# Kernel optimization log

Hardware: AMD Instinct MI355X
Metric: run time of the kernel (lower is better)

## Reference

```python
import jax, jax.numpy as jnp
import numpy as np

K, NR, NT, D, NLAYER = 128, 1, 128, 1, 8
PMAX = float(np.power(10.0, 10.0 / 10.0))  # snr=10 dB
SIGMA = 1.0


def _cx(x):
    # [2, ...] real/imag-stacked -> complex
    return x[0] + 1j * x[1]


def _ct(x):
    # conjugate transpose on last two axes
    return jnp.conj(jnp.swapaxes(x, -1, -2))


def _layer(Vc, Hc, up1, up3, up4, wp1, wp3, vp1, vp2, vp4):
    # Vc: [K,Nt,d] complex, Hc: [K,Nr,Nt] complex; params complex, batched over K.
    cdt = Vc.dtype
    I_nr = jnp.eye(NR, dtype=cdt)
    I_d = jnp.eye(D, dtype=cdt)
    I_nt = jnp.eye(NT, dtype=cdt)
    # ---- A_update: A_i = sigma/Pmax * sum_j tr(V_j V_j^H) * I + H_i (sum_j V_j V_j^H) H_i^H
    tr_vv = jnp.einsum('knd,knd->', Vc, jnp.conj(Vc))          # complex scalar
    S = jnp.einsum('knd,kmd->nm', Vc, jnp.conj(Vc))            # [Nt,Nt]
    A = (SIGMA / PMAX) * tr_vv * I_nr + jnp.einsum('krt,tm,ksm->krs', Hc, S, jnp.conj(Hc))  # [K,Nr,Nr]
    # ---- U layer: A_inv_i = p1_i inv(A_i) + 0.01 p3_i ; U_i = A_inv_i H_i V_i + p4_i
    A_inv = up1 @ jnp.linalg.inv(A) + 0.01 * up3
    Un = A_inv @ Hc @ Vc + up4                                  # [K,Nr,d]
    # ---- E_update: E_i = I - U_i^H H_i V_i
    E = I_d - _ct(Un) @ Hc @ Vc                                 # [K,d,d]
    # ---- W layer: W_i = 0.1 p1_i inv(E_i) + 0.01 p3_i
    Wn = 0.1 * (wp1 @ jnp.linalg.inv(E)) + 0.01 * wp3           # [K,d,d]
    # ---- B_update: B = sigma/Pmax * sum_i tr(U_i W_i U_i^H) * I + sum_i H_i^H U_i W_i U_i^H H_i (same for all users)
    UWU = Un @ Wn @ _ct(Un)                                     # [K,Nr,Nr]
    tr_uwu = jnp.trace(UWU, axis1=-2, axis2=-1).sum()
    B = (SIGMA / PMAX) * tr_uwu * I_nt + jnp.sum(_ct(Hc) @ UWU @ Hc, axis=0)  # [Nt,Nt]
    B_inv = jnp.linalg.inv(B)
    # ---- V
    if vp2 is None:  # FinalV: V_i = inv(B) H_i^H U_i W_i
        Vn = (B_inv @ _ct(Hc)) @ Un @ Wn
    else:            # V layer: B_inv_i = p2_i inv(B) + 0.01 p4_i ; V_i = B_inv_i H_i^H U_i W_i + p1_i
        Bm = vp2 @ B_inv + 0.01 * vp4
        Vn = Bm @ _ct(Hc) @ Un @ Wn + vp1
    # ---- Normalize: scale by sqrt(Pmax)/sqrt(Re sum_j tr(V_j V_j^H))
    pw = jnp.sqrt(jnp.real(jnp.einsum('knd,knd->', Vn, jnp.conj(Vn))))
    return (jnp.sqrt(PMAX) / pw) * Vn


def setup_inputs() -> dict:
    key = jax.random.key(0)
    ks = jax.random.split(key, 20)
    f32 = jnp.float32
    def rn(k, shape, scale):
        return (scale * jax.random.normal(k, shape)).astype(f32)
    inp = {
        'V': rn(ks[0], (2, K, NT, D), 1.0),
        'H': rn(ks[1], (2, K, NR, NT), 1.0),
        # mid-layer params, stacked over layers: only params actually used in forward
        'mid_u_p1': rn(ks[2], (NLAYER, 2, K, NR, NR), 0.001),
        'mid_u_p3': rn(ks[3], (NLAYER, 2, K, NR, NR), 0.01),
        'mid_u_p4': rn(ks[4], (NLAYER, 2, K, NR, D), 0.01),
        'mid_w_p1': rn(ks[5], (NLAYER, 2, K, D, D), 0.001),
        'mid_w_p3': rn(ks[6], (NLAYER, 2, K, D, D), 0.01),
        'mid_v_p1': rn(ks[7], (NLAYER, 2, K, NT, D), 0.001),
        'mid_v_p2': rn(ks[8], (NLAYER, 2, K, NT, NT), 0.01),
        'mid_v_p4': rn(ks[9], (NLAYER, 2, K, NT, NT), 0.01),
        # final layer (U + W only)
        'fin_u_p1': rn(ks[10], (2, K, NR, NR), 0.001),
        'fin_u_p3': rn(ks[11], (2, K, NR, NR), 0.01),
        'fin_u_p4': rn(ks[12], (2, K, NR, D), 0.01),
        'fin_w_p1': rn(ks[13], (2, K, D, D), 0.001),
        'fin_w_p3': rn(ks[14], (2, K, D, D), 0.01),
    }
    return inp


def reference(V, H, mid_u_p1, mid_u_p3, mid_u_p4, mid_w_p1, mid_w_p3,
              mid_v_p1, mid_v_p2, mid_v_p4,
              fin_u_p1, fin_u_p3, fin_u_p4, fin_w_p1, fin_w_p3):
    Vc = _cx(V)
    Hc = _cx(H)
    n = mid_u_p1.shape[0]
    for l in range(n):
        Vc = _layer(Vc, Hc,
                    _cx(mid_u_p1[l]), _cx(mid_u_p3[l]), _cx(mid_u_p4[l]),
                    _cx(mid_w_p1[l]), _cx(mid_w_p3[l]),
                    _cx(mid_v_p1[l]), _cx(mid_v_p2[l]), _cx(mid_v_p4[l]))
    Vc = _layer(Vc, Hc,
                _cx(fin_u_p1), _cx(fin_u_p3), _cx(fin_u_p4),
                _cx(fin_w_p1), _cx(fin_w_p3), None, None, None)
    return jnp.stack([jnp.real(Vc), jnp.imag(Vc)]).astype(jnp.float32)
```

## Files before the change

kernel.cpp:

```cpp
#include <hip/hip_runtime.h>
#include <math.h>

#define KK 128
#define NTT 128
#define PMAXF 10.0f
#define SP 0.1f
#define LDA2 130

typedef float2 c32;

__device__ __forceinline__ c32 cmul(c32 a, c32 b){
    return make_float2(a.x*b.x - a.y*b.y, a.x*b.y + a.y*b.x);
}
__device__ __forceinline__ c32 cmulc(c32 a, c32 b){
    return make_float2(a.x*b.x + a.y*b.y, a.y*b.x - a.x*b.y);
}
__device__ __forceinline__ c32 cinv(c32 a){
    float d = 1.0f/(a.x*a.x + a.y*a.y);
    return make_float2(a.x*d, -a.y*d);
}

__global__ void k_trvv(const float* __restrict__ V0, float* __restrict__ out){
    float s = 0.f;
    for (int e = blockIdx.x*blockDim.x + threadIdx.x; e < 2*KK*NTT; e += gridDim.x*blockDim.x){
        float v = V0[e]; s += v*v;
    }
    __shared__ float red[4];
    for (int d = 32; d; d >>= 1) s += __shfl_down(s, d);
    int lane = threadIdx.x & 63, w = threadIdx.x >> 6;
    if (!lane) red[w] = s;
    __syncthreads();
    if (!threadIdx.x){
        float t = red[0] + red[1] + red[2] + red[3];
        atomicAdd(out, t);
    }
}

__global__ void k_stage1(const float* __restrict__ Hre, const float* __restrict__ Him,
                         const float* __restrict__ V0re, const float* __restrict__ V0im,
                         const float2* __restrict__ VN, int use_vn,
                         const float* __restrict__ pw2prev,
                         const float* __restrict__ trvvp,
                         const float* __restrict__ u1, const float* __restrict__ u3,
                         const float* __restrict__ u4, const float* __restrict__ w1,
                         const float* __restrict__ w3,
                         float* __restrict__ wre, float* __restrict__ wim,
                         float* __restrict__ sre, float* __restrict__ sim,
                         float* __restrict__ sumw)
{
    int k = blockIdx.x, j = threadIdx.x;
    __shared__ float hre_s[NTT], him_s[NTT];
    __shared__ float redq[NTT];
    __shared__ c32 pkk_s;
    hre_s[j] = Hre[k*NTT + j];
    him_s[j] = Him[k*NTT + j];
    __syncthreads();

    float g = 1.0f;
    if (pw2prev) g = sqrtf(PMAXF / *pw2prev);

    float pre = 0.f, pim = 0.f;
    if (use_vn){
        const float2* vr = VN + j*NTT;
        #pragma unroll 4
        for (int n = 0; n < NTT; n++){
            float2 v = vr[n];
            pre += hre_s[n]*v.x - him_s[n]*v.y;
            pim += hre_s[n]*v.y + him_s[n]*v.x;
        }
    } else {
        const float* vr = V0re + j*NTT;
        const float* vi = V0im + j*NTT;
        #pragma unroll 4
        for (int n = 0; n < NTT; n++){
            float a = vr[n], b = vi[n];
            pre += hre_s[n]*a - him_s[n]*b;
            pim += hre_s[n]*b + him_s[n]*a;
        }
    }
    pre *= g; pim *= g;
    if (j == k) pkk_s = make_float2(pre, pim);
    redq[j] = pre*pre + pim*pim;
    __syncthreads();
    for (int d = 64; d; d >>= 1){
        if (j < d) redq[j] += redq[j + d];
        __syncthreads();
    }
    if (j == 0){
        float trvv = pw2prev ? PMAXF : *trvvp;
        float A = SP*trvv + redq[0];
        float invA = 1.0f/A;
        c32 p1 = make_float2(u1[k], u1[KK + k]);
        c32 p3 = make_float2(u3[k], u3[KK + k]);
        c32 p4 = make_float2(u4[k], u4[KK + k]);
        c32 Ainv = make_float2(p1.x*invA + 0.01f*p3.x, p1.y*invA + 0.01f*p3.y);
        c32 Pkk = pkk_s;
        c32 U = cmul(Ainv, Pkk); U.x += p4.x; U.y += p4.y;
        c32 t = cmulc(Pkk, U);
        c32 E = make_float2(1.0f - t.x, -t.y);
        c32 iE = cinv(E);
        c32 q1 = make_float2(w1[k], w1[KK + k]);
        c32 q3 = make_float2(w3[k], w3[KK + k]);
        c32 W = cmul(q1, iE);
        W.x = 0.1f*W.x + 0.01f*q3.x;
        W.y = 0.1f*W.y + 0.01f*q3.y;
        float u2 = U.x*U.x + U.y*U.y;
        c32 wk = make_float2(u2*W.x, u2*W.y);
        c32 sk = cmul(U, W);
        wre[k] = wk.x; wim[k] = wk.y;
        sre[k] = sk.x; sim[k] = sk.y;
        atomicAdd(&sumw[0], wk.x);
        atomicAdd(&sumw[1], wk.y);
    }
}

__global__ void k_bbuild(const float* __restrict__ Hre, const float* __restrict__ Him,
                         const float* __restrict__ wre, const float* __restrict__ wim,
                         const float* __restrict__ sumw, float2* __restrict__ B)
{
    int n = blockIdx.x, m = threadIdx.x;
    __shared__ float cr[KK], ci[KK];
    {
        int k = m;
        c32 h = make_float2(Hre[k*NTT + n], -Him[k*NTT + n]);
        c32 wk = make_float2(wre[k], wim[k]);
        c32 t = cmul(h, wk);
        cr[k] = t.x; ci[k] = t.y;
    }
    __syncthreads();
    float br = 0.f, bi = 0.f;
    #pragma unroll 4
    for (int k = 0; k < KK; k++){
        float hr = Hre[k*NTT + m], hi = Him[k*NTT + m];
        br += cr[k]*hr - ci[k]*hi;
        bi += cr[k]*hi + ci[k]*hr;
    }
    if (n == m){ br += SP*sumw[0]; bi += SP*sumw[1]; }
    B[n*NTT + m] = make_float2(br, bi);
}

__global__ void __launch_bounds__(512, 1) k_lu12(const float2* __restrict__ B,
                                                 float2* __restrict__ BT,
                                                 float2* __restrict__ rcg,
                                                 int* __restrict__ permg,
                                                 const float* __restrict__ p4re,
                                                 const float* __restrict__ p4im,
                                                 const float* __restrict__ Hre,
                                                 const float* __restrict__ Him,
                                                 float2* __restrict__ Z)
{
    if (blockIdx.x > 0){
        int k = blockIdx.x - 1;
        int t = threadIdx.x;
        int r = t >> 2, q = t & 3;
        const float* mre = p4re + (size_t)k*16384 + (size_t)r*128 + q*32;
        const float* mim = p4im + (size_t)k*16384 + (size_t)r*128 + q*32;
        const float* hr4 = Hre + k*NTT + q*32;
        const float* hi4 = Him + k*NTT + q*32;
        float ar = 0.f, ai = 0.f;
        #pragma unroll
        for (int ii = 0; ii < 8; ++ii){
            float4 a = *(const float4*)(mre + 4*ii);
            float4 b = *(const float4*)(mim + 4*ii);
            float4 hr = *(const float4*)(hr4 + 4*ii);
            float4 hi = *(const float4*)(hi4 + 4*ii);
            ar += a.x*hr.x + b.x*hi.x;  ai += b.x*hr.x - a.x*hi.x;
            ar += a.y*hr.y + b.y*hi.y;  ai += b.y*hr.y - a.y*hi.y;
            ar += a.z*hr.z + b.z*hi.z;  ai += b.z*hr.z - a.z*hi.z;
            ar += a.w*hr.w + b.w*hi.w;  ai += b.w*hr.w - a.w*hi.w;
        }
        ar += __shfl_xor(ar, 1); ai += __shfl_xor(ai, 1);
        ar += __shfl_xor(ar, 2); ai += __shfl_xor(ai, 2);
        if (q == 0) Z[k*NTT + r] = make_float2(ar, ai);
        return;
    }

    extern __shared__ float2 As[];
    __shared__ float2 rc_s[KK];
    __shared__ float2 Us[16*17];
    __shared__ float2 MM[16*16];
    __shared__ float2 MscT[16*114];
    const int t = threadIdx.x;

    {
        const float4* B4 = (const float4*)B;
        float4* A4 = (float4*)As;
        for (int e = t; e < KK*64; e += 512){
            int r = e >> 6, cq = e & 63;
            A4[r*65 + cq] = B4[e];
        }
    }
    __syncthreads();

    for (int j = 0; j < 8; ++j){
        const int J0 = j*16, T0 = J0 + 16, Rt = 128 - T0;

        if (t < 64){
            if (t < 16){
                const int l = t;
                float2 d[16], rcr[16];
                #pragma unroll
                for (int h = 0; h < 8; ++h){
                    float4 q = *(const float4*)&As[(J0 + l)*LDA2 + J0 + 2*h];
                    d[2*h]   = make_float2(q.x, q.y);
                    d[2*h+1] = make_float2(q.z, q.w);
                }
                #pragma unroll
                for (int ii = 0; ii < 16; ++ii){
                    float2 piv;
                    piv.x = __shfl(d[ii].x, ii);
                    piv.y = __shfl(d[ii].y, ii);
                    float2 rc = cinv(piv);
                    rcr[ii] = rc;
                    if (l == ii) rc_s[J0 + ii] = rc;
                    float2 m = cmul(d[ii], rc);
                    const bool act = (l > ii);
                    #pragma unroll
                    for (int c = ii + 1; c < 16; ++c){
                        float ux = __shfl(d[c].x, ii);
                        float uy = __shfl(d[c].y, ii);
                        if (act){
                            d[c].x -= m.x*ux - m.y*uy;
                            d[c].y -= m.x*uy + m.y*ux;
                        }
                    }
                }
                #pragma unroll
                for (int h = 0; h < 8; ++h)
                    *(float4*)&As[(J0 + l)*LDA2 + J0 + 2*h] =
                        make_float4(d[2*h].x, d[2*h].y, d[2*h+1].x, d[2*h+1].y);
                #pragma unroll
                for (int c = 0; c < 16; ++c) Us[l*17 + c] = d[c];
                if (l >= 1){
                    #pragma unroll
                    for (int i = 0; i < 15; ++i){
                        if (i < l) MM[l*16 + i] = cmul(d[i], rcr[i]);
                    }
                }
            }
        } else if (j > 0){
            const int J0p = J0 - 16;
            const int ncp = (128 - T0) >> 1;
            int tt = t - 64;
            int cp = tt & 63, g = tt >> 6;
            if (cp < ncp){
                int c0 = T0 + 2*cp;
                float4 u2[16];
                #pragma unroll
                for (int i = 0; i < 16; ++i)
                    u2[i] = *(const float4*)&As[(J0p + i)*LDA2 + c0];
                int nb = (128 - J0) >> 1;
                for (int rb = g; rb < nb; rb += 7){
                    int r0_ = J0 + 2*rb;
                    float4 a0_ = *(const float4*)&As[r0_*LDA2 + c0];
                    float4 a1_ = *(const float4*)&As[(r0_ + 1)*LDA2 + c0];
                    #pragma unroll
                    for (int i = 0; i < 16; ++i){
                        float4 mm = *(const float4*)&MscT[i*114 + 2*rb];
                        float4 u = u2[i];
                        a0_.x -= mm.x*u.x - mm.y*u.y;  a0_.y -= mm.x*u.y + mm.y*u.x;
                        a0_.z -= mm.x*u.z - mm.y*u.w;  a0_.w -= mm.x*u.w + mm.y*u.z;
                        a1_.x -= mm.z*u.x - mm.w*u.y;  a1_.y -= mm.z*u.y + mm.w*u.x;
                        a1_.z -= mm.z*u.z - mm.w*u.w;  a1_.w -= mm.z*u.w + mm.w*u.z;
                    }
                    *(float4*)&As[r0_*LDA2 + c0] = a0_;
                    *(float4*)&As[(r0_ + 1)*LDA2 + c0] = a1_;
                }
            }
        }
        __syncthreads();

        if (j == 7) break;

        if (t < Rt){
            int c = T0 + t;
            float2 u[16];
            #pragma unroll
            for (int i = 0; i < 16; ++i) u[i] = As[(J0 + i)*LDA2 + c];
            #pragma unroll
            for (int a2 = 1; a2 < 16; ++a2){
                #pragma unroll
                for (int i = 0; i < 16; ++i){
                    if (i < a2){
                        float2 mm = MM[a2*16 + i];
                        u[a2].x -= mm.x*u[i].x - mm.y*u[i].y;
                        u[a2].y -= mm.x*u[i].y + mm.y*u[i].x;
                    }
                }
            }
            #pragma unroll
            for (int a2 = 1; a2 < 16; ++a2) As[(J0 + a2)*LDA2 + c] = u[a2];
        } else if (t >= 256 && t < 256 + Rt){
            int r = T0 + (t - 256);
            float2 v[16], tv[16];
            #pragma unroll
            for (int h = 0; h < 8; ++h){
                float4 q = *(const float4*)&As[r*LDA2 + J0 + 2*h];
                v[2*h]   = make_float2(q.x, q.y);
                v[2*h+1] = make_float2(q.z, q.w);
            }
            #pragma unroll
            for (int c = 0; c < 16; ++c){
                #pragma unroll
                for (int i = 0; i < 16; ++i){
                    if (i < c){
                        float2 uu = Us[i*17 + c];
                        float2 ti = tv[i];
                        v[c].x -= ti.x*uu.x - ti.y*uu.y;
                        v[c].y -= ti.x*uu.y + ti.y*uu.x;
                    }
                }
                tv[c] = cmul(v[c], rc_s[J0 + c]);
            }
            #pragma unroll
            for (int h = 0; h < 8; ++h)
                *(float4*)&As[r*LDA2 + J0 + 2*h] =
                    make_float4(v[2*h].x, v[2*h].y, v[2*h+1].x, v[2*h+1].y);
            int rp = r - T0;
            #pragma unroll
            for (int i = 0; i < 16; ++i) MscT[i*114 + rp] = tv[i];
        }
        __syncthreads();

        {
            int cp = t & 7, g = t >> 3;
            int c0 = T0 + 2*cp;
            float4 u2[16];
            #pragma unroll
            for (int i = 0; i < 16; ++i)
                u2[i] = *(const float4*)&As[(J0 + i)*LDA2 + c0];
            int nb = Rt >> 1;
            for (int rb = g; rb < nb; rb += 64){
                int r0_ = T0 + 2*rb;
                float4 a0_ = *(const float4*)&As[r0_*LDA2 + c0];
                float4 a1_ = *(const float4*)&As[(r0_ + 1)*LDA2 + c0];
                #pragma unroll
                for (int i = 0; i < 16; ++i){
                    float4 mm = *(const float4*)&MscT[i*114 + 2*rb];
                    float4 u = u2[i];
                    a0_.x -= mm.x*u.x - mm.y*u.y;  a0_.y -= mm.x*u.y + mm.y*u.x;
                    a0_.z -= mm.x*u.z - mm.y*u.w;  a0_.w -= mm.x*u.w + mm.y*u.z;
                    a1_.x -= mm.z*u.x - mm.w*u.y;  a1_.y -= mm.z*u.y + mm.w*u.x;
                    a1_.z -= mm.z*u.z - mm.w*u.w;  a1_.w -= mm.z*u.w + mm.w*u.z;
                }
                *(float4*)&As[r0_*LDA2 + c0] = a0_;
                *(float4*)&As[(r0_ + 1)*LDA2 + c0] = a1_;
            }
        }
        __syncthreads();
    }

    for (int e = t; e < KK*NTT; e += 512){
        int c = e >> 7, r = e & 127;
        BT[e] = As[r*LDA2 + c];
    }
    if (t < KK){ rcg[t] = rc_s[t]; permg[t] = t; }
}

__device__ __forceinline__ void solve_col(const float2* __restrict__ BT,
                                          const float2* __restrict__ rc_s,
                                          const int* __restrict__ permg,
                                          const float* __restrict__ Hre,
                                          const float* __restrict__ Him,
                                          int c, int lane, float2* __restrict__ xv)
{
    int r0 = lane, r1 = lane + 64;
    int o0 = permg[r0], o1 = permg[r1];
    float2 b0 = make_float2(Hre[c*NTT + o0], -Him[c*NTT + o0]);
    float2 b1 = make_float2(Hre[c*NTT + o1], -Him[c*NTT + o1]);

    float2 cur0[8], cur1[8];
    #pragma unroll
    for (int jj = 0; jj < 8; jj++){ cur0[jj] = BT[jj*NTT + r0]; cur1[jj] = BT[jj*NTT + r1]; }
    for (int ib = 0; ib < 16; ib++){
        float2 n0[8], n1[8];
        if (ib < 15){
            int nb = (ib + 1)*8;
            #pragma unroll
            for (int jj = 0; jj < 8; jj++){ n0[jj] = BT[(nb + jj)*NTT + r0]; n1[jj] = BT[(nb + jj)*NTT + r1]; }
        }
        #pragma unroll
        for (int jj = 0; jj < 8; jj++){
            int i = ib*8 + jj;
            float xr, xi;
            if (i < 64){ xr = __shfl(b0.x, i);      xi = __shfl(b0.y, i); }
            else       { xr = __shfl(b1.x, i - 64); xi = __shfl(b1.y, i - 64); }
            float2 rc = rc_s[i];
            float tr = rc.x*xr - rc.y*xi, ti = rc.x*xi + rc.y*xr;
            float2 l0 = cur0[jj], l1 = cur1[jj];
            if (r0 > i){ b0.x -= l0.x*tr - l0.y*ti; b0.y -= l0.x*ti + l0.y*tr; }
            if (r1 > i){ b1.x -= l1.x*tr - l1.y*ti; b1.y -= l1.x*ti + l1.y*tr; }
        }
        if (ib < 15){
            #pragma unroll
            for (int jj = 0; jj < 8; jj++){ cur0[jj] = n0[jj]; cur1[jj] = n1[jj]; }
        }
    }
    #pragma unroll
    for (int jj = 0; jj < 8; jj++){ cur0[jj] = BT[(120 + jj)*NTT + r0]; cur1[jj] = BT[(120 + jj)*NTT + r1]; }
    for (int ib = 15; ib >= 0; ib--){
        float2 n0[8], n1[8];
        if (ib > 0){
            int nb = (ib - 1)*8;
            #pragma unroll
            for (int jj = 0; jj < 8; jj++){ n0[jj] = BT[(nb + jj)*NTT + r0]; n1[jj] = BT[(nb + jj)*NTT + r1]; }
        }
        #pragma unroll
        for (int jj = 7; jj >= 0; jj--){
            int i = ib*8 + jj;
            float yr, yi;
            if (i < 64){ yr = __shfl(b0.x, i);      yi = __shfl(b0.y, i); }
            else       { yr = __shfl(b1.x, i - 64); yi = __shfl(b1.y, i - 64); }
            float2 rc = rc_s[i];
            float xr = rc.x*yr - rc.y*yi, xi = rc.x*yi + rc.y*yr;
            if (r0 == i){ b0.x = xr; b0.y = xi; }
            if (r1 == i){ b1.x = xr; b1.y = xi; }
            float2 u0 = cur0[jj], u1v = cur1[jj];
            if (r0 < i){ b0.x -= u0.x*xr - u0.y*xi; b0.y -= u0.x*xi + u0.y*xr; }
            if (r1 < i){ b1.x -= u1v.x*xr - u1v.y*xi; b1.y -= u1v.x*xi + u1v.y*xr; }
        }
        if (ib > 0){
            #pragma unroll
            for (int jj = 0; jj < 8; jj++){ cur0[jj] = n0[jj]; cur1[jj] = n1[jj]; }
        }
    }
    xv[r0] = b0;
    xv[r1] = b1;
}

__global__ void __launch_bounds__(512) k_solvemv(const float2* __restrict__ BT,
                                                 const float2* __restrict__ rcg,
                                                 const int* __restrict__ permg,
                                                 const float* __restrict__ Hre, const float* __restrict__ Him,
                                                 const float* __restrict__ p2re, const float* __restrict__ p2im,
                                                 const float2* __restrict__ Z,
                                                 const float* __restrict__ sre, const float* __restrict__ sim,
                                                 const float* __restrict__ p1re, const float* __restrict__ p1im,
                                                 float2* __restrict__ VN, float* __restrict__ pw2)
{
    int k = blockIdx.x;
    int t = threadIdx.x;
    __shared__ float2 xv[NTT];
    __shared__ float2 rc_s[KK];
    __shared__ float red[8];

    int r = t >> 2, q = t & 3;
    const float* mre = p2re + (size_t)k*16384 + (size_t)r*128 + q*32;
    const float* mim = p2im + (size_t)k*16384 + (size_t)r*128 + q*32;
    float4 pa[8], pb[8];
    #pragma unroll
    for (int ii = 0; ii < 8; ++ii){
        pa[ii] = *(const float4*)(mre + 4*ii);
        pb[ii] = *(const float4*)(mim + 4*ii);
    }
    if (t < 64){
        rc_s[t] = rcg[t];
        rc_s[t + 64] = rcg[t + 64];
        solve_col(BT, rc_s, permg, Hre, Him, k, t, xv);
    }
    __syncthreads();

    float ar = 0.f, ai = 0.f;
    #pragma unroll
    for (int ii = 0; ii < 8; ++ii){
        float4 a = pa[ii], b = pb[ii];
        float2 x0 = xv[q*32 + 4*ii], x1 = xv[q*32 + 4*ii + 1];
        float2 x2 = xv[q*32 + 4*ii + 2], x3 = xv[q*32 + 4*ii + 3];
        ar += a.x*x0.x - b.x*x0.y;  ai += a.x*x0.y + b.x*x0.x;
        ar += a.y*x1.x - b.y*x1.y;  ai += a.y*x1.y + b.y*x1.x;
        ar += a.z*x2.x - b.z*x2.y;  ai += a.z*x2.y + b.z*x2.x;
        ar += a.w*x3.x - b.w*x3.y;  ai += a.w*x3.y + b.w*x3.x;
    }
    ar += __shfl_xor(ar, 1); ai += __shfl_xor(ai, 1);
    ar += __shfl_xor(ar, 2); ai += __shfl_xor(ai, 2);
    float pwl = 0.f;
    if (q == 0){
        float2 z = Z[k*NTT + r];
        c32 s = make_float2(sre[k], sim[k]);
        float2 y = make_float2(ar + 0.01f*z.x, ai + 0.01f*z.y);
        c32 v = cmul(s, y);
        v.x += p1re[k*NTT + r]; v.y += p1im[k*NTT + r];
        VN[k*NTT + r] = v;
        pwl = v.x*v.x + v.y*v.y;
    }
    for (int d = 32; d; d >>= 1) pwl += __shfl_down(pwl, d);
    int lane = t & 63, w = t >> 6;
    if (!lane) red[w] = pwl;
    __syncthreads();
    if (!t){
        float tt = 0.f;
        #pragma unroll
        for (int w2 = 0; w2 < 8; ++w2) tt += red[w2];
        atomicAdd(pw2, tt);
    }
}

__global__ void __launch_bounds__(64) k_solvefin(const float2* __restrict__ BT,
                                                 const float2* __restrict__ rcg,
                                                 const int* __restrict__ permg,
                                                 const float* __restrict__ Hre, const float* __restrict__ Him,
                                                 const float* __restrict__ sre, const float* __restrict__ sim,
                                                 float2* __restrict__ VN, float* __restrict__ pw2)
{
    int c = blockIdx.x;
    int lane = threadIdx.x;
    __shared__ float2 xv[NTT];
    __shared__ float2 rc_s[KK];
    rc_s[lane] = rcg[lane];
    rc_s[lane + 64] = rcg[lane + 64];
    solve_col(BT, rc_s, permg, Hre, Him, c, lane, xv);

    c32 s = make_float2(sre[c], sim[c]);
    float2 v0 = cmul(s, xv[lane]);
    float2 v1 = cmul(s, xv[lane + 64]);
    VN[c*NTT + lane] = v0;
    VN[c*NTT + lane + 64] = v1;
    float pwl = v0.x*v0.x + v0.y*v0.y + v1.x*v1.x + v1.y*v1.y;
    for (int d = 32; d; d >>= 1) pwl += __shfl_down(pwl, d);
    if (!lane) atomicAdd(pw2, pwl);
}

__global__ void k_write(const float2* __restrict__ VN, const float* __restrict__ pw2,
                        float* __restrict__ out)
{
    float gsc = sqrtf(PMAXF / *pw2);
    for (int e = blockIdx.x*blockDim.x + threadIdx.x; e < KK*NTT; e += gridDim.x*blockDim.x){
        float2 v = VN[e];
        out[e] = gsc*v.x;
        out[KK*NTT + e] = gsc*v.y;
    }
}

extern "C" void kernel_launch(void* const* d_in, const int* in_sizes, int n_in,
                              void* d_out, int out_size, void* d_ws, size_t ws_size,
                              hipStream_t stream)
{
    const float* V0  = (const float*)d_in[0];
    const float* H   = (const float*)d_in[1];
    const float* mu1 = (const float*)d_in[2];
    const float* mu3 = (const float*)d_in[3];
    const float* mu4 = (const float*)d_in[4];
    const float* mw1 = (const float*)d_in[5];
    const float* mw3 = (const float*)d_in[6];
    const float* mv1 = (const float*)d_in[7];
    const float* mv2 = (const float*)d_in[8];
    const float* mv4 = (const float*)d_in[9];
    const float* fu1 = (const float*)d_in[10];
    const float* fu3 = (const float*)d_in[11];
    const float* fu4 = (const float*)d_in[12];
    const float* fw1 = (const float*)d_in[13];
    const float* fw3 = (const float*)d_in[14];

    float* ws = (float*)d_ws;
    float*  acc  = ws;
    float*  wre  = ws + 64;
    float*  wim  = ws + 192;
    float*  sre  = ws + 320;
    float*  sim  = ws + 448;
    float2* B    = (float2*)(ws + 1024);
    float2* rc   = (float2*)(ws + 33792);
    int*    perm = (int*)  (ws + 34048);
    float2* Z    = (float2*)(ws + 99712);
    float2* VN   = (float2*)(ws + 132480);
    float2* BT   = (float2*)(ws + 165248);

    const int LU_LDS = KK*LDA2*sizeof(float2);
    (void)hipFuncSetAttribute((const void*)k_lu12,
                              hipFuncAttributeMaxDynamicSharedMemorySize, LU_LDS);

    hipMemsetAsync(ws, 0, 64*sizeof(float), stream);
    k_trvv<<<64, 256, 0, stream>>>(V0, ws + 40);

    const float* Hre = H;
    const float* Him = H + 16384;

    for (int l = 0; l < 9; l++){
        bool fin = (l == 8);
        const float* u1 = fin ? fu1 : mu1 + (size_t)l*256;
        const float* u3 = fin ? fu3 : mu3 + (size_t)l*256;
        const float* u4 = fin ? fu4 : mu4 + (size_t)l*256;
        const float* w1 = fin ? fw1 : mw1 + (size_t)l*256;
        const float* w3 = fin ? fw3 : mw3 + (size_t)l*256;

        k_stage1<<<128, 128, 0, stream>>>(Hre, Him, V0, V0 + 16384, VN, (l > 0) ? 1 : 0,
                                          (l > 0) ? (acc + (l - 1)*4 + 2) : nullptr,
                                          ws + 40,
                                          u1, u3, u4, w1, w3,
                                          wre, wim, sre, sim, acc + l*4);
        k_bbuild<<<128, 128, 0, stream>>>(Hre, Him, wre, wim, acc + l*4, B);

        if (!fin){
            const float* p4 = mv4 + (size_t)l*4194304;
            k_lu12<<<129, 512, LU_LDS, stream>>>(B, BT, rc, perm,
                                                 p4, p4 + 2097152, Hre, Him, Z);
            const float* p2 = mv2 + (size_t)l*4194304;
            const float* p1 = mv1 + (size_t)l*32768;
            k_solvemv<<<128, 512, 0, stream>>>(BT, rc, perm, Hre, Him,
                                               p2, p2 + 2097152, Z,
                                               sre, sim, p1, p1 + 16384,
                                               VN, acc + l*4 + 2);
        } else {
            k_lu12<<<1, 512, LU_LDS, stream>>>(B, BT, rc, perm,
                                               nullptr, nullptr, Hre, Him, Z);
            k_solvefin<<<128, 64, 0, stream>>>(BT, rc, perm, Hre, Him,
                                               sre, sim, VN, acc + l*4 + 2);
            k_write<<<64, 256, 0, stream>>>(VN, acc + l*4 + 2, (float*)d_out);
        }
    }
}
```

Measured before the change: 1.548 ms.

## Move Z precompute out of LU kernel and overlap with previous layer's solve

Measured after the change: 1.555 ms. No clear change (+0.5%).

```diff
diff --git a/kernel.cpp b/kernel.cpp
--- a/kernel.cpp
+++ b/kernel.cpp
@@ -50,7 +50,7 @@
 {
     int k = blockIdx.x, j = threadIdx.x;
     __shared__ float hre_s[NTT], him_s[NTT];
-    __shared__ float redq[NTT];
+    __shared__ float red2[2];
     __shared__ c32 pkk_s;
     hre_s[j] = Hre[k*NTT + j];
     him_s[j] = Him[k*NTT + j];
@@ -80,15 +80,15 @@
     }
     pre *= g; pim *= g;
     if (j == k) pkk_s = make_float2(pre, pim);
-    redq[j] = pre*pre + pim*pim;
+    float q = pre*pre + pim*pim;
+    #pragma unroll
+    for (int d = 32; d; d >>= 1) q += __shfl_down(q, d);
+    if ((j & 63) == 0) red2[j >> 6] = q;
     __syncthreads();
-    for (int d = 64; d; d >>= 1){
-        if (j < d) redq[j] += redq[j + d];
-        __syncthreads();
-    }
     if (j == 0){
+        float qq = red2[0] + red2[1];
         float trvv = pw2prev ? PMAXF : *trvvp;
-        float A = SP*trvv + redq[0];
+        float A = SP*trvv + qq;
         float invA = 1.0f/A;
         c32 p1 = make_float2(u1[k], u1[KK + k]);
         c32 p3 = make_float2(u3[k], u3[KK + k]);
@@ -139,42 +139,49 @@
     B[n*NTT + m] = make_float2(br, bi);
 }
 
-__global__ void __launch_bounds__(512, 1) k_lu12(const float2* __restrict__ B,
+__device__ __forceinline__ void z_body(int k, int t,
+                                       const float* __restrict__ p4re,
+                                       const float* __restrict__ p4im,
+                                       const float* __restrict__ Hre,
+                                       const float* __restrict__ Him,
+                                       float2* __restrict__ Z)
+{
+    int r = t >> 2, q = t & 3;
+    const float* mre = p4re + (size_t)k*16384 + (size_t)r*128 + q*32;
+    const float* mim = p4im + (size_t)k*16384 + (size_t)r*128 + q*32;
+    const float* hr4 = Hre + k*NTT + q*32;
+    const float* hi4 = Him + k*NTT + q*32;
+    float ar = 0.f, ai = 0.f;
+    #pragma unroll
+    for (int ii = 0; ii < 8; ++ii){
+        float4 a = *(const float4*)(mre + 4*ii);
+        float4 b = *(const float4*)(mim + 4*ii);
+        float4 hr = *(const float4*)(hr4 + 4*ii);
+        float4 hi = *(const float4*)(hi4 + 4*ii);
+        ar += a.x*hr.x + b.x*hi.x;  ai += b.x*hr.x - a.x*hi.x;
+        ar += a.y*hr.y + b.y*hi.y;  ai += b.y*hr.y - a.y*hi.y;
+        ar += a.z*hr.z + b.z*hi.z;  ai += b.z*hr.z - a.z*hi.z;
+        ar += a.w*hr.w + b.w*hi.w;  ai += b.w*hr.w - a.w*hi.w;
+    }
+    ar += __shfl_xor(ar, 1); ai += __shfl_xor(ai, 1);
+    ar += __shfl_xor(ar, 2); ai += __shfl_xor(ai, 2);
+    if (q == 0) Z[k*NTT + r] = make_float2(ar, ai);
+}
+
+__global__ void __launch_bounds__(512) k_z(const float* __restrict__ p4re,
+                                           const float* __restrict__ p4im,
+                                           const float* __restrict__ Hre,
+                                           const float* __restrict__ Him,
+                                           float2* __restrict__ Z)
+{
+    z_body(blockIdx.x, threadIdx.x, p4re, p4im, Hre, Him, Z);
+}
+
+__global__ void __launch_bounds__(512, 1) k_lu14(const float2* __restrict__ B,
                                                  float2* __restrict__ BT,
                                                  float2* __restrict__ rcg,
-                                                 int* __restrict__ permg,
-                                                 const float* __restrict__ p4re,
-                                                 const float* __restrict__ p4im,
-                                                 const float* __restrict__ Hre,
-                                                 const float* __restrict__ Him,
-                                                 float2* __restrict__ Z)
-{
-    if (blockIdx.x > 0){
-        int k = blockIdx.x - 1;
-        int t = threadIdx.x;
-        int r = t >> 2, q = t & 3;
-        const float* mre = p4re + (size_t)k*16384 + (size_t)r*128 + q*32;
-        const float* mim = p4im + (size_t)k*16384 + (size_t)r*128 + q*32;
-        const float* hr4 = Hre + k*NTT + q*32;
-        const float* hi4 = Him + k*NTT + q*32;
-        float ar = 0.f, ai = 0.f;
-        #pragma unroll
-        for (int ii = 0; ii < 8; ++ii){
-            float4 a = *(const float4*)(mre + 4*ii);
-            float4 b = *(const float4*)(mim + 4*ii);
-            float4 hr = *(const float4*)(hr4 + 4*ii);
-            float4 hi = *(const float4*)(hi4 + 4*ii);
-            ar += a.x*hr.x + b.x*hi.x;  ai += b.x*hr.x - a.x*hi.x;
-            ar += a.y*hr.y + b.y*hi.y;  ai += b.y*hr.y - a.y*hi.y;
-            ar += a.z*hr.z + b.z*hi.z;  ai += b.z*hr.z - a.z*hi.z;
-            ar += a.w*hr.w + b.w*hi.w;  ai += b.w*hr.w - a.w*hi.w;
-        }
-        ar += __shfl_xor(ar, 1); ai += __shfl_xor(ai, 1);
-        ar += __shfl_xor(ar, 2); ai += __shfl_xor(ai, 2);
-        if (q == 0) Z[k*NTT + r] = make_float2(ar, ai);
-        return;
-    }
-
+                                                 int* __restrict__ permg)
+{
     extern __shared__ float2 As[];
     __shared__ float2 rc_s[KK];
     __shared__ float2 Us[16*17];
@@ -433,11 +440,17 @@
                                                  const int* __restrict__ permg,
                                                  const float* __restrict__ Hre, const float* __restrict__ Him,
                                                  const float* __restrict__ p2re, const float* __restrict__ p2im,
-                                                 const float2* __restrict__ Z,
+                                                 const float2* __restrict__ Zcur,
                                                  const float* __restrict__ sre, const float* __restrict__ sim,
                                                  const float* __restrict__ p1re, const float* __restrict__ p1im,
-                                                 float2* __restrict__ VN, float* __restrict__ pw2)
-{
+                                                 float2* __restrict__ VN, float* __restrict__ pw2,
+                                                 const float* __restrict__ p4nre, const float* __restrict__ p4nim,
+                                                 float2* __restrict__ Znext)
+{
+    if (blockIdx.x >= 128){
+        if (p4nre) z_body(blockIdx.x - 128, threadIdx.x, p4nre, p4nim, Hre, Him, Znext);
+        return;
+    }
     int k = blockIdx.x;
     int t = threadIdx.x;
     __shared__ float2 xv[NTT];
@@ -475,7 +488,7 @@
     ar += __shfl_xor(ar, 2); ai += __shfl_xor(ai, 2);
     float pwl = 0.f;
     if (q == 0){
-        float2 z = Z[k*NTT + r];
+        float2 z = Zcur[k*NTT + r];
         c32 s = make_float2(sre[k], sim[k]);
         float2 y = make_float2(ar + 0.01f*z.x, ai + 0.01f*z.y);
         c32 v = cmul(s, y);
@@ -560,12 +573,13 @@
     float2* B    = (float2*)(ws + 1024);
     float2* rc   = (float2*)(ws + 33792);
     int*    perm = (int*)  (ws + 34048);
-    float2* Z    = (float2*)(ws + 99712);
+    float2* Zb1  = (float2*)(ws + 34176);
+    float2* Zb0  = (float2*)(ws + 99712);
     float2* VN   = (float2*)(ws + 132480);
     float2* BT   = (float2*)(ws + 165248);
 
     const int LU_LDS = KK*LDA2*sizeof(float2);
-    (void)hipFuncSetAttribute((const void*)k_lu12,
+    (void)hipFuncSetAttribute((const void*)k_lu14,
                               hipFuncAttributeMaxDynamicSharedMemorySize, LU_LDS);
 
     hipMemsetAsync(ws, 0, 64*sizeof(float), stream);
@@ -573,6 +587,8 @@
 
     const float* Hre = H;
     const float* Him = H + 16384;
+
+    k_z<<<128, 512, 0, stream>>>(mv4, mv4 + 2097152, Hre, Him, Zb0);
 
     for (int l = 0; l < 9; l++){
         bool fin = (l == 8);
@@ -588,20 +604,20 @@
                                           u1, u3, u4, w1, w3,
                                           wre, wim, sre, sim, acc + l*4);
         k_bbuild<<<128, 128, 0, stream>>>(Hre, Him, wre, wim, acc + l*4, B);
+        k_lu14<<<1, 512, LU_LDS, stream>>>(B, BT, rc, perm);
 
         if (!fin){
-            const float* p4 = mv4 + (size_t)l*4194304;
-            k_lu12<<<129, 512, LU_LDS, stream>>>(B, BT, rc, perm,
-                                                 p4, p4 + 2097152, Hre, Him, Z);
             const float* p2 = mv2 + (size_t)l*4194304;
             const float* p1 = mv1 + (size_t)l*32768;
-            k_solvemv<<<128, 512, 0, stream>>>(BT, rc, perm, Hre, Him,
-                                               p2, p2 + 2097152, Z,
+            float2* Zcur  = (l & 1) ? Zb1 : Zb0;
+            float2* Znext = (l & 1) ? Zb0 : Zb1;
+            const float* p4n = (l + 1 < 8) ? (mv4 + (size_t)(l + 1)*4194304) : nullptr;
+            k_solvemv<<<256, 512, 0, stream>>>(BT, rc, perm, Hre, Him,
+                                               p2, p2 + 2097152, Zcur,
                                                sre, sim, p1, p1 + 16384,
-                                               VN, acc + l*4 + 2);
+                                               VN, acc + l*4 + 2,
+                                               p4n, p4n ? (p4n + 2097152) : nullptr, Znext);
         } else {
-            k_lu12<<<1, 512, LU_LDS, stream>>>(B, BT, rc, perm,
-                                               nullptr, nullptr, Hre, Him, Z);
             k_solvefin<<<128, 64, 0, stream>>>(BT, rc, perm, Hre, Him,
                                                sre, sim, VN, acc + l*4 + 2);
             k_write<<<64, 256, 0, stream>>>(VN, acc + l*4 + 2, (float*)d_out);
```
